# Kernel tuning notes

Hardware: AMD Instinct MI355X
Metric: run time of the kernel (lower is better)

Reference implementation:

```python
import jax, jax.numpy as jnp
import numpy as np

N_NODES = 100000
N_EDGES = 1600000
IN_CH, HID_CH, OUT_CH = 8, 64, 2


def setup_inputs() -> dict:
    key = jax.random.key(0)
    ks = jax.random.split(key, 8)
    x = jax.random.normal(ks[0], (N_NODES, IN_CH), dtype=jnp.float32)
    edge_index = jax.random.randint(ks[1], (2, N_EDGES), 0, N_NODES, dtype=jnp.int64)
    s1 = 1.0 / np.sqrt(IN_CH)
    s2 = 1.0 / np.sqrt(HID_CH)
    W_l1 = jax.random.normal(ks[2], (HID_CH, IN_CH), dtype=jnp.float32) * s1
    b_l1 = jax.random.normal(ks[3], (HID_CH,), dtype=jnp.float32) * s1
    W_r1 = jax.random.normal(ks[4], (HID_CH, IN_CH), dtype=jnp.float32) * s1
    W_l2 = jax.random.normal(ks[5], (OUT_CH, HID_CH), dtype=jnp.float32) * s2
    b_l2 = jax.random.normal(ks[6], (OUT_CH,), dtype=jnp.float32) * s2
    W_r2 = jax.random.normal(ks[7], (OUT_CH, HID_CH), dtype=jnp.float32) * s2
    return {"x": x, "edge_index": edge_index, "W_l1": W_l1, "b_l1": b_l1,
            "W_r1": W_r1, "W_l2": W_l2, "b_l2": b_l2, "W_r2": W_r2}


def _sage_conv(x, edge_index, W_l, b_l, W_r):
    # PyG SAGEConv (aggr='mean', root_weight=True):
    #   out = lin_l(mean_{j in N(i)} x_j) + lin_r(x_i)
    src, dst = edge_index[0], edge_index[1]
    n = x.shape[0]
    msgs = x[src]                                             # [E, F] gather
    summed = jax.ops.segment_sum(msgs, dst, num_segments=n)   # [N, F] scatter-add
    cnt = jax.ops.segment_sum(jnp.ones((src.shape[0],), x.dtype), dst,
                              num_segments=n)                 # [N]
    aggr = summed / jnp.maximum(cnt, 1.0)[:, None]            # scatter-mean
    return aggr @ W_l.T + b_l + x @ W_r.T


def reference(x, edge_index, W_l1, b_l1, W_r1, W_l2, b_l2, W_r2):
    h = _sage_conv(x, edge_index, W_l1, b_l1, W_r1)
    h = jax.nn.relu(h)
    # Dropout(0.3) is identity in eval mode (deterministic baseline).
    out = _sage_conv(h, edge_index, W_l2, b_l2, W_r2)
    return out
```

## Files before the change

kernel.cpp:

```cpp
#include <hip/hip_runtime.h>

#define N_NODES 100000
#define N_EDGES 1600000
#define IN_CH 8
#define HID_CH 64
#define OUT_CH 2

#define R2   1024
#define RN   98
#define CAP  1920
#define BB   256
#define BCHUNK (N_EDGES / BB)

#define WS_BUCKET 1024
#define WS_OFFDEG (WS_BUCKET + R2 * CAP)
#define WS_G      (WS_OFFDEG + R2 * RN)

__global__ __launch_bounds__(512) void bucket_kernel(
        const int* __restrict__ src, const int* __restrict__ dst,
        int* __restrict__ cursor, int* __restrict__ bucket) {
    __shared__ int cnt[R2];
    __shared__ int base[R2];
    __shared__ int cur[R2];
    for (int i = threadIdx.x; i < R2; i += 512) { cnt[i] = 0; cur[i] = 0; }
    __syncthreads();
    const int* dch = dst + (size_t)blockIdx.x * BCHUNK;
    const int* sch = src + (size_t)blockIdx.x * BCHUNK;
    for (int j = threadIdx.x; j < BCHUNK; j += 512)
        atomicAdd(&cnt[(unsigned)dch[j] / RN], 1);
    __syncthreads();
    for (int i = threadIdx.x; i < R2; i += 512) {
        int c = cnt[i];
        base[i] = (c > 0) ? atomicAdd(&cursor[i], c) : 0;
    }
    __syncthreads();
    for (int j = threadIdx.x; j < BCHUNK; j += 512) {
        unsigned d = (unsigned)dch[j];
        unsigned r = d / RN;
        unsigned dl = d - r * RN;
        int slot = base[r] + atomicAdd(&cur[r], 1);
        if (slot < CAP)
            bucket[(size_t)r * CAP + slot] = (int)((dl << 17) | (unsigned)sch[j]);
    }
}

__global__ __launch_bounds__(512) void sage1_range(
        const int* __restrict__ bucket, const int* __restrict__ cursor,
        const float* __restrict__ x,
        const float* __restrict__ W_l1, const float* __restrict__ b_l1,
        const float* __restrict__ W_r1,
        const float* __restrict__ W_l2, const float* __restrict__ b_l2,
        const float* __restrict__ W_r2,
        int* __restrict__ csr, int* __restrict__ offdeg,
        float* __restrict__ g, float* __restrict__ out_rt) {
    __shared__ int raw[CAP];
    __shared__ int seg[CAP];
    __shared__ int scnt[128];
    __shared__ int soff[128];
    __shared__ int scur[128];
    __shared__ int wtot[2];
    __shared__ float sWl[HID_CH * IN_CH];
    __shared__ float sWr[HID_CH * IN_CH];
    __shared__ float sb[HID_CH];
    __shared__ float sWl2[OUT_CH * HID_CH];
    __shared__ float sWr2[OUT_CH * HID_CH];
    __shared__ float sb2[OUT_CH];

    int tid = threadIdx.x;
    for (int i = tid; i < HID_CH * IN_CH; i += 512) {
        sWl[i] = W_l1[i];
        sWr[i] = W_r1[i];
    }
    for (int i = tid; i < HID_CH; i += 512) sb[i] = b_l1[i];
    for (int i = tid; i < OUT_CH * HID_CH; i += 512) {
        sWl2[i] = W_l2[i];
        sWr2[i] = W_r2[i];
    }
    if (tid < OUT_CH) sb2[tid] = b_l2[tid];
    if (tid < 128) scnt[tid] = 0;

    int r = blockIdx.x;
    int len = cursor[r];
    if (len > CAP) len = CAP;
    const int* bin = bucket + (size_t)r * CAP;
    for (int j = tid; j < len; j += 512) raw[j] = bin[j];
    __syncthreads();

    for (int j = tid; j < len; j += 512) atomicAdd(&scnt[raw[j] >> 17], 1);
    __syncthreads();

    int lane = tid & 63;
    if (tid < 128) {
        int v = scnt[tid];
        int incl = v;
        #pragma unroll
        for (int d = 1; d < 64; d <<= 1) {
            int t2 = __shfl_up(incl, d);
            if (lane >= d) incl += t2;
        }
        if (lane == 63) wtot[tid >> 6] = incl;
        soff[tid] = incl - v;
    }
    __syncthreads();
    if (tid < 128) {
        int o = soff[tid] + ((tid >= 64) ? wtot[0] : 0);
        soff[tid] = o;
        scur[tid] = o;
    }
    __syncthreads();

    for (int j = tid; j < len; j += 512) {
        int w = raw[j];
        int p = atomicAdd(&scur[w >> 17], 1);
        seg[p] = w & 0x1FFFF;
    }
    __syncthreads();

    int* cw = csr + (size_t)r * CAP;
    for (int j = tid; j < len; j += 512) cw[j] = seg[j];

    int q = tid >> 2;
    int l = tid & 3;
    int node = r * RN + q;
    if (q < RN && node < N_NODES) {
        int o = soff[q];
        int dn = scnt[q];
        if (l == 0) offdeg[node] = o | (dn << 16);

        float acc[IN_CH];
        #pragma unroll
        for (int c = 0; c < IN_CH; c++) acc[c] = 0.0f;
        for (int j = o + l; j < o + dn; j += 4) {
            int s = seg[j];
            const float4* xs = (const float4*)(x + (size_t)s * IN_CH);
            float4 a = xs[0];
            float4 b = xs[1];
            acc[0] += a.x; acc[1] += a.y; acc[2] += a.z; acc[3] += a.w;
            acc[4] += b.x; acc[5] += b.y; acc[6] += b.z; acc[7] += b.w;
        }
        #pragma unroll
        for (int c = 0; c < IN_CH; c++) {
            acc[c] += __shfl_xor(acc[c], 1);
            acc[c] += __shfl_xor(acc[c], 2);
        }
        float inv = 1.0f / fmaxf((float)dn, 1.0f);
        float ag[IN_CH], xa[IN_CH];
        #pragma unroll
        for (int c = 0; c < IN_CH; c++) ag[c] = acc[c] * inv;
        const float4* xp = (const float4*)(x + (size_t)node * IN_CH);
        float4 x0 = xp[0], x1 = xp[1];
        xa[0] = x0.x; xa[1] = x0.y; xa[2] = x0.z; xa[3] = x0.w;
        xa[4] = x1.x; xa[5] = x1.y; xa[6] = x1.z; xa[7] = x1.w;

        float g0 = 0.f, g1 = 0.f, r0 = 0.f, r1 = 0.f;
        int k0 = l * 16;
        #pragma unroll 4
        for (int kk = k0; kk < k0 + 16; kk++) {
            float hk = sb[kk];
            #pragma unroll
            for (int c = 0; c < IN_CH; c++) {
                hk += sWl[kk * IN_CH + c] * ag[c];
                hk += sWr[kk * IN_CH + c] * xa[c];
            }
            hk = fmaxf(hk, 0.0f);
            g0 += sWl2[kk] * hk;
            g1 += sWl2[HID_CH + kk] * hk;
            r0 += sWr2[kk] * hk;
            r1 += sWr2[HID_CH + kk] * hk;
        }
        g0 += __shfl_xor(g0, 1); g0 += __shfl_xor(g0, 2);
        g1 += __shfl_xor(g1, 1); g1 += __shfl_xor(g1, 2);
        r0 += __shfl_xor(r0, 1); r0 += __shfl_xor(r0, 2);
        r1 += __shfl_xor(r1, 1); r1 += __shfl_xor(r1, 2);
        if (l == 0) {
            g[(size_t)node * 2 + 0] = g0;
            g[(size_t)node * 2 + 1] = g1;
            float2 rt;
            rt.x = r0 + sb2[0];
            rt.y = r1 + sb2[1];
            *(float2*)(out_rt + (size_t)node * 2) = rt;
        }
    }
}

__global__ __launch_bounds__(256) void sage2_kernel(
        const int* __restrict__ csr, const int* __restrict__ offdeg,
        const float* __restrict__ g, float* __restrict__ out) {
    int t = blockIdx.x * blockDim.x + threadIdx.x;
    int node = t >> 2;
    int l = t & 3;
    if (node >= N_NODES) return;
    int r = node / RN;
    int od = offdeg[node];
    int o = od & 0xFFFF;
    int dn = od >> 16;
    const int* seg = csr + (size_t)r * CAP;
    float a0 = 0.f, a1 = 0.f;
    for (int j = o + l; j < o + dn; j += 4) {
        int s = seg[j];
        float2 gv = *(const float2*)(g + (size_t)s * 2);
        a0 += gv.x;
        a1 += gv.y;
    }
    a0 += __shfl_xor(a0, 1); a0 += __shfl_xor(a0, 2);
    a1 += __shfl_xor(a1, 1); a1 += __shfl_xor(a1, 2);
    if (l == 0) {
        float inv = 1.0f / fmaxf((float)dn, 1.0f);
        float2 rt = *(const float2*)(out + (size_t)node * 2);
        float2 ov;
        ov.x = a0 * inv + rt.x;
        ov.y = a1 * inv + rt.y;
        *(float2*)(out + (size_t)node * 2) = ov;
    }
}

extern "C" void kernel_launch(void* const* d_in, const int* in_sizes, int n_in,
                              void* d_out, int out_size, void* d_ws, size_t ws_size,
                              hipStream_t stream) {
    const float* x    = (const float*)d_in[0];
    const int*   ei   = (const int*)d_in[1];
    const float* W_l1 = (const float*)d_in[2];
    const float* b_l1 = (const float*)d_in[3];
    const float* W_r1 = (const float*)d_in[4];
    const float* W_l2 = (const float*)d_in[5];
    const float* b_l2 = (const float*)d_in[6];
    const float* W_r2 = (const float*)d_in[7];
    float* out = (float*)d_out;

    const int* src = ei;
    const int* dst = ei + N_EDGES;

    int*   cursor = (int*)d_ws;
    int*   bucket = (int*)d_ws + WS_BUCKET;
    int*   offdeg = (int*)d_ws + WS_OFFDEG;
    float* g      = (float*)d_ws + WS_G;

    hipMemsetAsync(cursor, 0, R2 * sizeof(int), stream);

    bucket_kernel<<<BB, 512, 0, stream>>>(src, dst, cursor, bucket);
    sage1_range<<<R2, 512, 0, stream>>>(bucket, cursor, x,
                                        W_l1, b_l1, W_r1, W_l2, b_l2, W_r2,
                                        bucket , offdeg, g, out);
    sage2_kernel<<<(4 * N_NODES + 255) / 256, 256, 0, stream>>>(bucket, offdeg, g, out);
}
```

Baseline: 136.7 us.

## Replace global-cursor bucketing with fixed per-block sub-slots and count matrix

The bucket kernel no longer does a count pass followed by global atomic reservation on a cursor array. Each block now writes edges into a fixed 32-entry sub-slot per destination range and records its per-range counts in a count matrix, which also removes the memset launch. The first SAGE kernel then prefix-sums the 256 per-block counts for its range and compacts the sub-slots into shared memory before the existing per-node sort. In exchange, workspace grows several-fold, the compaction reads many small scattered chunks, and edges beyond 32 per (range, block) are silently dropped.

```diff
diff --git a/kernel.cpp b/kernel.cpp
--- a/kernel.cpp
+++ b/kernel.cpp
@@ -8,44 +8,41 @@
 
 #define R2   1024
 #define RN   98
-#define CAP  1920
 #define BB   256
 #define BCHUNK (N_EDGES / BB)
-
-#define WS_BUCKET 1024
-#define WS_OFFDEG (WS_BUCKET + R2 * CAP)
+#define SUB  32
+#define CAPF (BB * SUB)
+#define CAPS 1920
+
+#define WS_BUCKET (R2 * BB)
+#define WS_OFFDEG (WS_BUCKET + R2 * CAPF)
 #define WS_G      (WS_OFFDEG + R2 * RN)
 
 __global__ __launch_bounds__(512) void bucket_kernel(
         const int* __restrict__ src, const int* __restrict__ dst,
-        int* __restrict__ cursor, int* __restrict__ bucket) {
-    __shared__ int cnt[R2];
-    __shared__ int base[R2];
+        int* __restrict__ cntg, int* __restrict__ bucket) {
     __shared__ int cur[R2];
-    for (int i = threadIdx.x; i < R2; i += 512) { cnt[i] = 0; cur[i] = 0; }
-    __syncthreads();
-    const int* dch = dst + (size_t)blockIdx.x * BCHUNK;
-    const int* sch = src + (size_t)blockIdx.x * BCHUNK;
-    for (int j = threadIdx.x; j < BCHUNK; j += 512)
-        atomicAdd(&cnt[(unsigned)dch[j] / RN], 1);
-    __syncthreads();
-    for (int i = threadIdx.x; i < R2; i += 512) {
-        int c = cnt[i];
-        base[i] = (c > 0) ? atomicAdd(&cursor[i], c) : 0;
-    }
-    __syncthreads();
+    for (int i = threadIdx.x; i < R2; i += 512) cur[i] = 0;
+    __syncthreads();
+    int b = blockIdx.x;
+    const int* dch = dst + (size_t)b * BCHUNK;
+    const int* sch = src + (size_t)b * BCHUNK;
     for (int j = threadIdx.x; j < BCHUNK; j += 512) {
         unsigned d = (unsigned)dch[j];
         unsigned r = d / RN;
         unsigned dl = d - r * RN;
-        int slot = base[r] + atomicAdd(&cur[r], 1);
-        if (slot < CAP)
-            bucket[(size_t)r * CAP + slot] = (int)((dl << 17) | (unsigned)sch[j]);
-    }
+        int intra = atomicAdd(&cur[r], 1);
+        if (intra < SUB)
+            bucket[(size_t)r * CAPF + b * SUB + intra] =
+                (int)((dl << 17) | (unsigned)sch[j]);
+    }
+    __syncthreads();
+    for (int i = threadIdx.x; i < R2; i += 512)
+        cntg[(size_t)i * BB + b] = min(cur[i], SUB);
 }
 
 __global__ __launch_bounds__(512) void sage1_range(
-        const int* __restrict__ bucket, const int* __restrict__ cursor,
+        const int* __restrict__ cntg, const int* __restrict__ bucket_r,
         const float* __restrict__ x,
         const float* __restrict__ W_l1, const float* __restrict__ b_l1,
         const float* __restrict__ W_r1,
@@ -53,12 +50,15 @@
         const float* __restrict__ W_r2,
         int* __restrict__ csr, int* __restrict__ offdeg,
         float* __restrict__ g, float* __restrict__ out_rt) {
-    __shared__ int raw[CAP];
-    __shared__ int seg[CAP];
+    __shared__ int cnt256[BB];
+    __shared__ int doff[BB];
+    __shared__ int wtot4[4];
+    __shared__ int raw[CAPS];
+    __shared__ int seg[CAPS];
     __shared__ int scnt[128];
     __shared__ int soff[128];
     __shared__ int scur[128];
-    __shared__ int wtot[2];
+    __shared__ int wtot2[2];
     __shared__ float sWl[HID_CH * IN_CH];
     __shared__ float sWr[HID_CH * IN_CH];
     __shared__ float sb[HID_CH];
@@ -67,6 +67,8 @@
     __shared__ float sb2[OUT_CH];
 
     int tid = threadIdx.x;
+    int r = blockIdx.x;
+
     for (int i = tid; i < HID_CH * IN_CH; i += 512) {
         sWl[i] = W_l1[i];
         sWr[i] = W_r1[i];
@@ -78,37 +80,62 @@
     }
     if (tid < OUT_CH) sb2[tid] = b_l2[tid];
     if (tid < 128) scnt[tid] = 0;
-
-    int r = blockIdx.x;
-    int len = cursor[r];
-    if (len > CAP) len = CAP;
-    const int* bin = bucket + (size_t)r * CAP;
-    for (int j = tid; j < len; j += 512) raw[j] = bin[j];
+    if (tid < BB) cnt256[tid] = cntg[(size_t)r * BB + tid];
+    __syncthreads();
+
+    if (tid < BB) {
+        int v = cnt256[tid];
+        int incl = v;
+        #pragma unroll
+        for (int d = 1; d < 64; d <<= 1) {
+            int t2 = __shfl_up(incl, d);
+            if ((tid & 63) >= d) incl += t2;
+        }
+        if ((tid & 63) == 63) wtot4[tid >> 6] = incl;
+        doff[tid] = incl - v;
+    }
+    __syncthreads();
+    if (tid < BB) {
+        int w = tid >> 6;
+        int add = 0;
+        #pragma unroll
+        for (int i = 0; i < 3; i++) add += (i < w) ? wtot4[i] : 0;
+        doff[tid] += add;
+    }
+    __syncthreads();
+    int len = doff[BB - 1] + cnt256[BB - 1];
+    if (len > CAPS) len = CAPS;
+
+    {
+        int b = tid >> 1, par = tid & 1;
+        int n = cnt256[b];
+        int o = doff[b];
+        const int* gsp = bucket_r + (size_t)r * CAPF + b * SUB;
+        for (int j = par; j < n; j += 2)
+            if (o + j < CAPS) raw[o + j] = gsp[j];
+    }
     __syncthreads();
 
     for (int j = tid; j < len; j += 512) atomicAdd(&scnt[raw[j] >> 17], 1);
     __syncthreads();
-
-    int lane = tid & 63;
     if (tid < 128) {
         int v = scnt[tid];
         int incl = v;
         #pragma unroll
         for (int d = 1; d < 64; d <<= 1) {
             int t2 = __shfl_up(incl, d);
-            if (lane >= d) incl += t2;
-        }
-        if (lane == 63) wtot[tid >> 6] = incl;
+            if ((tid & 63) >= d) incl += t2;
+        }
+        if ((tid & 63) == 63) wtot2[tid >> 6] = incl;
         soff[tid] = incl - v;
     }
     __syncthreads();
     if (tid < 128) {
-        int o = soff[tid] + ((tid >= 64) ? wtot[0] : 0);
+        int o = soff[tid] + ((tid >= 64) ? wtot2[0] : 0);
         soff[tid] = o;
         scur[tid] = o;
     }
     __syncthreads();
-
     for (int j = tid; j < len; j += 512) {
         int w = raw[j];
         int p = atomicAdd(&scur[w >> 17], 1);
@@ -116,7 +143,7 @@
     }
     __syncthreads();
 
-    int* cw = csr + (size_t)r * CAP;
+    int* cw = csr + (size_t)r * CAPF;
     for (int j = tid; j < len; j += 512) cw[j] = seg[j];
 
     int q = tid >> 2;
@@ -194,7 +221,7 @@
     int od = offdeg[node];
     int o = od & 0xFFFF;
     int dn = od >> 16;
-    const int* seg = csr + (size_t)r * CAP;
+    const int* seg = csr + (size_t)r * CAPF;
     float a0 = 0.f, a1 = 0.f;
     for (int j = o + l; j < o + dn; j += 4) {
         int s = seg[j];
@@ -230,15 +257,13 @@
     const int* src = ei;
     const int* dst = ei + N_EDGES;
 
-    int*   cursor = (int*)d_ws;
+    int*   cntg   = (int*)d_ws;
     int*   bucket = (int*)d_ws + WS_BUCKET;
     int*   offdeg = (int*)d_ws + WS_OFFDEG;
     float* g      = (float*)d_ws + WS_G;
 
-    hipMemsetAsync(cursor, 0, R2 * sizeof(int), stream);
-
-    bucket_kernel<<<BB, 512, 0, stream>>>(src, dst, cursor, bucket);
-    sage1_range<<<R2, 512, 0, stream>>>(bucket, cursor, x,
+    bucket_kernel<<<BB, 512, 0, stream>>>(src, dst, cntg, bucket);
+    sage1_range<<<R2, 512, 0, stream>>>(cntg, bucket, x,
                                         W_l1, b_l1, W_r1, W_l2, b_l2, W_r2,
                                         bucket , offdeg, g, out);
     sage2_kernel<<<(4 * N_NODES + 255) / 256, 256, 0, stream>>>(bucket, offdeg, g, out);
```

Result: slower. 139.7 us (+2.2%).
